# Performance work log

Hardware: AMD Instinct MI355X
Metric: run time of the kernel (lower is better)

## Reference

```python
import jax, jax.numpy as jnp
import numpy as np

N_HEAD = 16
D_MODEL = 1024
D_K = 64
D_V = 64
LN_EPS = 1e-6


def setup_inputs() -> dict:
    key = jax.random.key(0)
    ks = jax.random.split(key, 10)
    B, S = 2, 2048
    scale = 0.02
    return {
        "q": jax.random.normal(ks[0], (B, S, D_MODEL), jnp.float32),
        "k": jax.random.normal(ks[1], (B, S, D_MODEL), jnp.float32),
        "v": jax.random.normal(ks[2], (B, S, D_MODEL), jnp.float32),
        "Wq": jax.random.normal(ks[3], (D_MODEL, N_HEAD * D_K), jnp.float32) * scale,
        "Wk": jax.random.normal(ks[4], (D_MODEL, N_HEAD * D_K), jnp.float32) * scale,
        "Wv": jax.random.normal(ks[5], (D_MODEL, N_HEAD * D_V), jnp.float32) * scale,
        "Wfc": jax.random.normal(ks[6], (N_HEAD * D_V, D_MODEL), jnp.float32) * scale,
        "bfc": jnp.zeros((D_MODEL,), jnp.float32),
        "gamma": jnp.ones((D_MODEL,), jnp.float32),
        "beta": jnp.zeros((D_MODEL,), jnp.float32),
    }


def reference(q, k, v, Wq, Wk, Wv, Wfc, bfc, gamma, beta):
    B, S, _ = q.shape
    residual = q
    # QKV projections, split into heads: [B, S, H, Dh]
    qh = (q @ Wq).reshape(B, S, N_HEAD, D_K)
    kh = (k @ Wk).reshape(B, S, N_HEAD, D_K)
    vh = (v @ Wv).reshape(B, S, N_HEAD, D_V)
    # scaled dot-product attention (explicit score matrix, as in source)
    temperature = jnp.asarray(D_K, qh.dtype) ** 0.5
    attn = jnp.einsum("bqhd,bkhd->bhqk", qh, kh) / temperature
    attn = jax.nn.softmax(attn, axis=-1)
    out = jnp.einsum("bhqk,bkhd->bqhd", attn, vh).reshape(B, S, N_HEAD * D_V)
    # output projection (dropout is identity in eval mode)
    out = out @ Wfc + bfc
    # residual + layernorm (eps=1e-6)
    x = out + residual
    mu = jnp.mean(x, axis=-1, keepdims=True)
    var = jnp.mean(jnp.square(x - mu), axis=-1, keepdims=True)
    return (x - mu) / jnp.sqrt(var + LN_EPS) * gamma + beta
```

## Files before the change

kernel.cpp:

```cpp
#include <hip/hip_runtime.h>

typedef float f32x4 __attribute__((ext_vector_type(4)));
typedef short short8 __attribute__((ext_vector_type(8)));
typedef short short4v __attribute__((ext_vector_type(4)));
typedef unsigned int uint2v __attribute__((ext_vector_type(2)));
typedef unsigned short ushort_t;

#define D_MODEL 1024
#define N_HEAD 16
#define SEQ 2048
#define BATCH 2
#define M_TOK 4096
#define HD 1024
#define NT 32
#define APANEL 131072
#define WPANEL 32768
#define QSCALE_L2E 0.1803368801111f

__device__ __forceinline__ ushort_t f2bf(float f) {
    union { float f; unsigned int u; } x; x.f = f;
    unsigned int r = x.u + 0x7fffu + ((x.u >> 16) & 1u);
    return (ushort_t)(r >> 16);
}

__device__ __forceinline__ void async_copy16(const ushort_t* gptr, ushort_t* lptr) {
    __builtin_amdgcn_global_load_lds(
        (const __attribute__((address_space(1))) unsigned int*)gptr,
        (__attribute__((address_space(3))) unsigned int*)lptr, 16, 0, 0);
}

__global__ __launch_bounds__(256) void prep_fused(const float* __restrict__ w0,
                                                  const float* __restrict__ w1,
                                                  const float* __restrict__ w2,
                                                  const float* __restrict__ w3,
                                                  ushort_t* __restrict__ o0,
                                                  ushort_t* __restrict__ o1,
                                                  ushort_t* __restrict__ o2,
                                                  ushort_t* __restrict__ o3,
                                                  const float* __restrict__ q,
                                                  const float* __restrict__ k,
                                                  const float* __restrict__ v,
                                                  ushort_t* __restrict__ qo,
                                                  ushort_t* __restrict__ ko,
                                                  ushort_t* __restrict__ vo) {
    const int z = blockIdx.z;
    const int tid = threadIdx.x;
    const int flat = blockIdx.x + 64 * blockIdx.y;
    if (z < 4) {
        if (flat >= 1024) return;
        const int C = D_MODEL;
        const float* in = (z == 0) ? w0 : (z == 1) ? w1 : (z == 2) ? w2 : w3;
        ushort_t* out = (z == 0) ? o0 : (z == 1) ? o1 : (z == 2) ? o2 : o3;
        __shared__ ushort_t t[32][33];
        int bc = (flat & 31) * 32, br = (flat >> 5) * 32;
        int tx = tid & 31, ty = tid >> 5;
        for (int i = ty; i < 32; i += 8)
            t[i][tx] = f2bf(in[(size_t)(br + i) * C + bc + tx]);
        __syncthreads();
        size_t pbase = (size_t)(br >> 5) * WPANEL;
        for (int i = ty; i < 32; i += 8)
            out[pbase + (size_t)(bc + i) * 32 + tx] = t[tx][i];
    } else {
        const float* s = (z == 4) ? q : (z == 5) ? k : v;
        ushort_t* d = (z == 4) ? qo : (z == 5) ? ko : vo;
        size_t i = ((size_t)flat * 256 + tid) * 8;
        int m = (int)(i >> 10), k0 = (int)(i & 1023);
        float4 a = *(const float4*)(s + i);
        float4 b = *(const float4*)(s + i + 4);
        ushort_t tmp[8] = {f2bf(a.x), f2bf(a.y), f2bf(a.z), f2bf(a.w),
                           f2bf(b.x), f2bf(b.y), f2bf(b.z), f2bf(b.w)};
        *(short8*)(d + (size_t)(k0 >> 5) * APANEL + (size_t)m * 32 + (k0 & 31)) = *(short8*)tmp;
    }
}

__global__ __launch_bounds__(256) void gemm_qkv(const ushort_t* __restrict__ qb,
                                                const ushort_t* __restrict__ kb,
                                                const ushort_t* __restrict__ vb,
                                                const ushort_t* __restrict__ wq,
                                                const ushort_t* __restrict__ wk,
                                                const ushort_t* __restrict__ wv,
                                                ushort_t* __restrict__ Qo,
                                                ushort_t* __restrict__ Ko,
                                                ushort_t* __restrict__ V4) {
    __shared__ ushort_t As[2][128 * 32];
    __shared__ ushort_t Bs[2][128 * 32];
    const int z = blockIdx.z;
    const ushort_t* A = (z == 0) ? qb : (z == 1) ? kb : vb;
    const ushort_t* Bt = (z == 0) ? wq : (z == 1) ? wk : wv;
    const int tid = threadIdx.x;
    const int wave = tid >> 6, lane = tid & 63;
    const int quad = lane >> 4, l16 = lane & 15;
    const int m0 = blockIdx.x * 128, n0 = blockIdx.y * 128;
    const int wm = (wave >> 1) * 64, wn = (wave & 1) * 64;
    const int N = D_MODEL;

    f32x4 acc[4][4];
    for (int i = 0; i < 4; ++i)
        for (int j = 0; j < 4; ++j) acc[i][j] = (f32x4){0.f, 0.f, 0.f, 0.f};

    for (int it = 0; it < 16; ++it) {
        __syncthreads();
        const ushort_t* Ap = A + (size_t)(it * 2) * APANEL + (size_t)m0 * 32;
        const ushort_t* Bp = Bt + (size_t)(it * 2) * WPANEL + (size_t)n0 * 32;
        #pragma unroll
        for (int hf = 0; hf < 2; ++hf) {
            #pragma unroll
            for (int c = 0; c < 2; ++c) {
                int off = (wave * 2 + c) * 512;
                async_copy16(Ap + hf * APANEL + off + lane * 8, &As[hf][off] + lane * 8);
                async_copy16(Bp + hf * WPANEL + off + lane * 8, &Bs[hf][off] + lane * 8);
            }
        }
        __syncthreads();
        short8 af[4][2], bfr[4][2];
        #pragma unroll
        for (int i = 0; i < 4; ++i)
            #pragma unroll
            for (int sk = 0; sk < 2; ++sk)
                af[i][sk] = *(const short8*)&As[sk][(wm + i * 16 + l16) * 32 + quad * 8];
        #pragma unroll
        for (int j = 0; j < 4; ++j)
            #pragma unroll
            for (int sk = 0; sk < 2; ++sk)
                bfr[j][sk] = *(const short8*)&Bs[sk][(wn + j * 16 + l16) * 32 + quad * 8];
        #pragma unroll
        for (int sk = 0; sk < 2; ++sk)
            #pragma unroll
            for (int i = 0; i < 4; ++i)
                #pragma unroll
                for (int j = 0; j < 4; ++j)
                    acc[i][j] = __builtin_amdgcn_mfma_f32_16x16x32_bf16(af[i][sk], bfr[j][sk], acc[i][j], 0, 0, 0);
    }
    if (z == 2) {
        const int tile64 = m0 + wm;
        const int b2 = tile64 >> 11;
        const int kt = (tile64 & 2047) >> 6;
        #pragma unroll
        for (int i = 0; i < 4; ++i)
            #pragma unroll
            for (int j = 0; j < 4; ++j) {
                int n = n0 + wn + j * 16 + l16;
                int h2 = n >> 6, d = n & 63;
                int quadR = (quad + ((n >> 2) & 3)) & 3;
                ushort_t tmp[4];
                #pragma unroll
                for (int r = 0; r < 4; ++r) tmp[r] = f2bf(acc[i][j][r]);
                size_t dst = ((((size_t)(h2 * 2 + b2) * NT + kt) * 4 + i) << 10) + d * 16 + quadR * 4;
                *(short4v*)&V4[dst] = *(short4v*)tmp;
            }
    } else {
        ushort_t* C = (z == 0) ? Qo : Ko;
        const float scale = (z == 0) ? QSCALE_L2E : 1.0f;
        #pragma unroll
        for (int i = 0; i < 4; ++i)
            #pragma unroll
            for (int j = 0; j < 4; ++j) {
                int n = n0 + wn + j * 16 + l16;
                #pragma unroll
                for (int r = 0; r < 4; ++r) {
                    int m = m0 + wm + i * 16 + quad * 4 + r;
                    C[(size_t)m * N + n] = f2bf(acc[i][j][r] * scale);
                }
            }
    }
}

__global__ __launch_bounds__(256) void gemm_fc(const ushort_t* __restrict__ A,
                                               const ushort_t* __restrict__ Bt,
                                               float* __restrict__ Cf,
                                               const float* __restrict__ bias,
                                               const float* __restrict__ resid) {
    __shared__ ushort_t As[2][128 * 32];
    __shared__ ushort_t Bs[2][64 * 32];
    const int tid = threadIdx.x;
    const int wave = tid >> 6, lane = tid & 63;
    const int quad = lane >> 4, l16 = lane & 15;
    const int m0 = blockIdx.x * 128, n0 = blockIdx.y * 64;
    const int N = D_MODEL;

    f32x4 acc[2][4];
    for (int i = 0; i < 2; ++i)
        for (int j = 0; j < 4; ++j) acc[i][j] = (f32x4){0.f, 0.f, 0.f, 0.f};

    for (int it = 0; it < 16; ++it) {
        __syncthreads();
        const ushort_t* Ap = A + (size_t)(it * 2) * APANEL + (size_t)m0 * 32;
        const ushort_t* Bp = Bt + (size_t)(it * 2) * WPANEL + (size_t)n0 * 32;
        #pragma unroll
        for (int c = 0; c < 4; ++c) {
            int g = wave * 4 + c;
            int sk = g >> 3, off = (g & 7) * 512;
            async_copy16(Ap + sk * APANEL + off + lane * 8, &As[sk][off] + lane * 8);
        }
        #pragma unroll
        for (int c = 0; c < 2; ++c) {
            int g = wave * 2 + c;
            int sk = g >> 2, off = (g & 3) * 512;
            async_copy16(Bp + sk * WPANEL + off + lane * 8, &Bs[sk][off] + lane * 8);
        }
        __syncthreads();
        short8 af[2][2], bfr[4][2];
        #pragma unroll
        for (int i = 0; i < 2; ++i)
            #pragma unroll
            for (int sk = 0; sk < 2; ++sk)
                af[i][sk] = *(const short8*)&As[sk][(wave * 32 + i * 16 + l16) * 32 + quad * 8];
        #pragma unroll
        for (int j = 0; j < 4; ++j)
            #pragma unroll
            for (int sk = 0; sk < 2; ++sk)
                bfr[j][sk] = *(const short8*)&Bs[sk][(j * 16 + l16) * 32 + quad * 8];
        #pragma unroll
        for (int sk = 0; sk < 2; ++sk)
            #pragma unroll
            for (int i = 0; i < 2; ++i)
                #pragma unroll
                for (int j = 0; j < 4; ++j)
                    acc[i][j] = __builtin_amdgcn_mfma_f32_16x16x32_bf16(af[i][sk], bfr[j][sk], acc[i][j], 0, 0, 0);
    }
    #pragma unroll
    for (int i = 0; i < 2; ++i)
        #pragma unroll
        for (int j = 0; j < 4; ++j) {
            int n = n0 + j * 16 + l16;
            #pragma unroll
            for (int r = 0; r < 4; ++r) {
                int m = m0 + wave * 32 + i * 16 + quad * 4 + r;
                Cf[(size_t)m * N + n] = acc[i][j][r] + bias[n] + resid[(size_t)m * N + n];
            }
        }
}

__global__ __launch_bounds__(256, 3) void attn64(const ushort_t* __restrict__ Qh,
                                                 const ushort_t* __restrict__ Kh,
                                                 const ushort_t* __restrict__ V4,
                                                 ushort_t* __restrict__ O) {
    __shared__ __align__(16) char smem[25600];
    const int tid = threadIdx.x;
    const int wave = tid >> 6, lane = tid & 63;
    const int quad = lane >> 4, l16 = lane & 15;
    const int h = blockIdx.x, b = blockIdx.y, qt = blockIdx.z;
    const size_t base = (size_t)b * SEQ * HD + h * 64;
    const ushort_t* Qb = Qh + base + (size_t)(qt * 64) * HD;
    const ushort_t* Kb = Kh + base;
    const ushort_t* Vg = V4 + (((size_t)(h * 2 + b) * NT * 4) + wave) * 1024 + lane * 8;

    ushort_t* Vw = (ushort_t*)smem + wave * 3072;
    float* lsb = (float*)(smem + 24576);

    short8 qf[4][2];
    #pragma unroll
    for (int nt = 0; nt < 4; ++nt)
        #pragma unroll
        for (int s = 0; s < 2; ++s)
            qf[nt][s] = *(const short8*)(Qb + (size_t)(nt * 16 + l16) * HD + s * 32 + quad * 8);

    f32x4 oacc[4][4];
    #pragma unroll
    for (int nt = 0; nt < 4; ++nt)
        #pragma unroll
        for (int dt = 0; dt < 4; ++dt) oacc[nt][dt] = (f32x4){0.f, 0.f, 0.f, 0.f};
    float lsum[4] = {0.f, 0.f, 0.f, 0.f};

    const ushort_t* Kr = Kb + (size_t)(wave * 16 + l16) * HD + quad * 8;
    ushort_t* VLd = Vw + lane * 8;

    short8 kfA[2], kfB[2];
    #pragma unroll
    for (int s = 0; s < 2; ++s) kfA[s] = *(const short8*)(Kr + s * 32);
    #pragma unroll
    for (int c = 0; c < 2; ++c) async_copy16(Vg + c * 512, VLd + c * 512);
    #pragma unroll
    for (int s = 0; s < 2; ++s) kfB[s] = *(const short8*)(Kr + (size_t)64 * HD + s * 32);
    #pragma unroll
    for (int c = 0; c < 2; ++c) async_copy16(Vg + 4096 + c * 512, VLd + 1024 + c * 512);

    ushort_t *s0 = Vw, *s1 = Vw + 1024, *s2 = Vw + 2048;
    const int rot = (l16 >> 2) & 3;

#define ATTN_STEP(KT, KF, SUSE, SPF, WAITIMM, DO_PF)                                         \
    {                                                                                        \
        __builtin_amdgcn_s_waitcnt(WAITIMM);                                                 \
        short4v vf[4];                                                                       \
        _Pragma("unroll")                                                                    \
        for (int dt = 0; dt < 4; ++dt)                                                       \
            vf[dt] = *(const short4v*)&(SUSE)[(dt * 16 + l16) * 16 + (((quad + rot) & 3) * 4)]; \
        f32x4 sacc[4];                                                                       \
        _Pragma("unroll")                                                                    \
        for (int nt = 0; nt < 4; ++nt) sacc[nt] = (f32x4){0.f, 0.f, 0.f, 0.f};               \
        _Pragma("unroll")                                                                    \
        for (int s = 0; s < 2; ++s)                                                          \
            _Pragma("unroll")                                                                \
            for (int nt = 0; nt < 4; ++nt)                                                   \
                sacc[nt] = __builtin_amdgcn_mfma_f32_16x16x32_bf16(KF[s], qf[nt][s],         \
                                                                   sacc[nt], 0, 0, 0);       \
        if (DO_PF) {                                                                         \
            _Pragma("unroll")                                                                \
            for (int s = 0; s < 2; ++s)                                                      \
                KF[s] = *(const short8*)(Kr + (size_t)((KT) + 2) * 64 * HD + s * 32);        \
            _Pragma("unroll")                                                                \
            for (int c = 0; c < 2; ++c)                                                      \
                async_copy16(Vg + (size_t)((KT) + 2) * 4096 + c * 512,                       \
                             (SPF) + lane * 8 + c * 512);                                    \
        }                                                                                    \
        short4v pf[4];                                                                       \
        _Pragma("unroll")                                                                    \
        for (int nt = 0; nt < 4; ++nt) {                                                     \
            float p0 = __builtin_amdgcn_exp2f(sacc[nt][0]);                                  \
            float p1 = __builtin_amdgcn_exp2f(sacc[nt][1]);                                  \
            float p2 = __builtin_amdgcn_exp2f(sacc[nt][2]);                                  \
            float p3 = __builtin_amdgcn_exp2f(sacc[nt][3]);                                  \
            lsum[nt] += (p0 + p1) + (p2 + p3);                                               \
            unsigned int lo, hi;                                                             \
            asm("v_cvt_pk_bf16_f32 %0, %1, %2" : "=v"(lo) : "v"(p0), "v"(p1));               \
            asm("v_cvt_pk_bf16_f32 %0, %1, %2" : "=v"(hi) : "v"(p2), "v"(p3));               \
            uint2v pk;                                                                       \
            pk.x = lo;                                                                       \
            pk.y = hi;                                                                       \
            pf[nt] = __builtin_bit_cast(short4v, pk);                                        \
        }                                                                                    \
        _Pragma("unroll")                                                                    \
        for (int nt = 0; nt < 4; ++nt)                                                       \
            _Pragma("unroll")                                                                \
            for (int dt = 0; dt < 4; ++dt)                                                   \
                oacc[nt][dt] = __builtin_amdgcn_mfma_f32_16x16x16bf16_1k(pf[nt], vf[dt],     \
                                                                         oacc[nt][dt],       \
                                                                         0, 0, 0);           \
    }

    for (int kt0 = 0; kt0 < 30; kt0 += 2) {
        ATTN_STEP(kt0,     kfA, s0, s2, 0x0F74, true);
        ATTN_STEP(kt0 + 1, kfB, s1, s0, 0x0F74, true);
        ushort_t* t = s0; s0 = s2; s2 = s1; s1 = t;
    }
    ATTN_STEP(30, kfA, s0, s2, 0x0F74, false);
    ATTN_STEP(31, kfB, s1, s0, 0x0F70, false);
#undef ATTN_STEP

    #pragma unroll
    for (int nt = 0; nt < 4; ++nt) {
        lsum[nt] += __shfl_xor(lsum[nt], 16, 64);
        lsum[nt] += __shfl_xor(lsum[nt], 32, 64);
    }
    if (quad == 0) {
        #pragma unroll
        for (int nt = 0; nt < 4; ++nt) lsb[wave * 64 + nt * 16 + l16] = lsum[nt];
    }
    __syncthreads();

    float* R = (float*)smem;
    #pragma unroll
    for (int w = 0; w < 4; ++w) {
        if (wave == w) {
            #pragma unroll
            for (int nt = 0; nt < 4; ++nt)
                #pragma unroll
                for (int dt = 0; dt < 4; ++dt)
                    #pragma unroll
                    for (int i = 0; i < 4; ++i) {
                        int idx = (nt * 16 + quad * 4 + i) * 66 + dt * 16 + l16;
                        if (w == 0) R[idx] = oacc[nt][dt][i];
                        else        R[idx] += oacc[nt][dt][i];
                    }
        }
        __syncthreads();
    }
    float inv[4];
    #pragma unroll
    for (int i = 0; i < 4; ++i) {
        int qrow = wave * 16 + quad * 4 + i;
        float t = lsb[qrow] + lsb[64 + qrow] + lsb[128 + qrow] + lsb[192 + qrow];
        inv[i] = 1.f / t;
    }
    #pragma unroll
    for (int i = 0; i < 4; ++i) {
        int qrow = wave * 16 + quad * 4 + i;
        size_t tok = (size_t)b * SEQ + qt * 64 + qrow;
        #pragma unroll
        for (int dt = 0; dt < 4; ++dt) {
            int d = dt * 16 + l16;
            size_t dst = (size_t)(h * 2 + (dt >> 1)) * APANEL + tok * 32 + (dt & 1) * 16 + l16;
            O[dst] = f2bf(R[qrow * 66 + d] * inv[i]);
        }
    }
}

__global__ __launch_bounds__(256) void ln_kernel(float* __restrict__ x,
                                                 const float* __restrict__ gamma,
                                                 const float* __restrict__ beta) {
    const int D = D_MODEL;
    float* xr = x + (size_t)blockIdx.x * D;
    const int tid = threadIdx.x;
    float4 v = *(const float4*)(xr + tid * 4);
    float s = v.x + v.y + v.z + v.w;
    float s2 = v.x * v.x + v.y * v.y + v.z * v.z + v.w * v.w;
    #pragma unroll
    for (int off = 1; off < 64; off <<= 1) {
        s += __shfl_xor(s, off, 64);
        s2 += __shfl_xor(s2, off, 64);
    }
    __shared__ float ws1[4], ws2[4];
    int wave = tid >> 6, lane = tid & 63;
    if (lane == 0) { ws1[wave] = s; ws2[wave] = s2; }
    __syncthreads();
    s = ws1[0] + ws1[1] + ws1[2] + ws1[3];
    s2 = ws2[0] + ws2[1] + ws2[2] + ws2[3];
    float mean = s * (1.f / D);
    float var = s2 * (1.f / D) - mean * mean;
    float rstd = rsqrtf(var + 1e-6f);
    float4 g = *(const float4*)(gamma + tid * 4);
    float4 bt = *(const float4*)(beta + tid * 4);
    float4 o;
    o.x = (v.x - mean) * rstd * g.x + bt.x;
    o.y = (v.y - mean) * rstd * g.y + bt.y;
    o.z = (v.z - mean) * rstd * g.z + bt.z;
    o.w = (v.w - mean) * rstd * g.w + bt.w;
    *(float4*)(xr + tid * 4) = o;
}

extern "C" void kernel_launch(void* const* d_in, const int* in_sizes, int n_in,
                              void* d_out, int out_size, void* d_ws, size_t ws_size,
                              hipStream_t stream) {
    const float* q = (const float*)d_in[0];
    const float* k = (const float*)d_in[1];
    const float* v = (const float*)d_in[2];
    const float* Wq = (const float*)d_in[3];
    const float* Wk = (const float*)d_in[4];
    const float* Wv = (const float*)d_in[5];
    const float* Wfc = (const float*)d_in[6];
    const float* bfc = (const float*)d_in[7];
    const float* gamma = (const float*)d_in[8];
    const float* beta = (const float*)d_in[9];
    float* out = (float*)d_out;

    char* ws = (char*)d_ws;
    const size_t MB = 1u << 20;
    ushort_t* WqT  = (ushort_t*)(ws + 0 * MB);
    ushort_t* WkT  = (ushort_t*)(ws + 2 * MB);
    ushort_t* WvT  = (ushort_t*)(ws + 4 * MB);
    ushort_t* WfcT = (ushort_t*)(ws + 6 * MB);
    ushort_t* qb   = (ushort_t*)(ws + 8 * MB);
    ushort_t* kb   = (ushort_t*)(ws + 16 * MB);
    ushort_t* vb   = (ushort_t*)(ws + 24 * MB);
    ushort_t* Qh   = (ushort_t*)(ws + 32 * MB);
    ushort_t* Kh   = (ushort_t*)(ws + 40 * MB);
    ushort_t* Vt   = (ushort_t*)(ws + 48 * MB);
    ushort_t* Oh   = (ushort_t*)(ws + 8 * MB);

    const int M = M_TOK, D = D_MODEL;
    prep_fused<<<dim3(64, 32, 7), 256, 0, stream>>>(
        Wq, Wk, Wv, Wfc, WqT, WkT, WvT, WfcT, q, k, v, qb, kb, vb);

    gemm_qkv<<<dim3(M / 128, D / 128, 3), 256, 0, stream>>>(qb, kb, vb, WqT, WkT, WvT, Qh, Kh, Vt);

    attn64<<<dim3(N_HEAD, BATCH, SEQ / 64), 256, 0, stream>>>(Qh, Kh, Vt, Oh);

    gemm_fc<<<dim3(M / 128, D / 64), 256, 0, stream>>>(Oh, WfcT, out, bfc, q);

    ln_kernel<<<M, 256, 0, stream>>>(out, gamma, beta);
}
```

Measured before the change: 230.7 us.

## Software-pipeline attention PV MFMA one tile behind softmax exponentials

```diff
diff --git a/kernel.cpp b/kernel.cpp
--- a/kernel.cpp
+++ b/kernel.cpp
@@ -278,13 +278,14 @@
     ushort_t *s0 = Vw, *s1 = Vw + 1024, *s2 = Vw + 2048;
     const int rot = (l16 >> 2) & 3;
 
-#define ATTN_STEP(KT, KF, SUSE, SPF, WAITIMM, DO_PF)                                         \
+    short4v vfA[4], vfB[4], pfA[4], pfB[4];
+
+#define ATTN_STEP(KT, KF, SUSE, SPF, WAITIMM, DO_PF, VFW, PFW, VFR, PFR, DO_PV)              \
     {                                                                                        \
         __builtin_amdgcn_s_waitcnt(WAITIMM);                                                 \
-        short4v vf[4];                                                                       \
         _Pragma("unroll")                                                                    \
         for (int dt = 0; dt < 4; ++dt)                                                       \
-            vf[dt] = *(const short4v*)&(SUSE)[(dt * 16 + l16) * 16 + (((quad + rot) & 3) * 4)]; \
+            VFW[dt] = *(const short4v*)&(SUSE)[(dt * 16 + l16) * 16 + (((quad + rot) & 3) * 4)]; \
         f32x4 sacc[4];                                                                       \
         _Pragma("unroll")                                                                    \
         for (int nt = 0; nt < 4; ++nt) sacc[nt] = (f32x4){0.f, 0.f, 0.f, 0.f};               \
@@ -303,7 +304,16 @@
                 async_copy16(Vg + (size_t)((KT) + 2) * 4096 + c * 512,                       \
                              (SPF) + lane * 8 + c * 512);                                    \
         }                                                                                    \
-        short4v pf[4];                                                                       \
+        if (DO_PV) {                                                                        \
+            _Pragma("unroll")                                                                \
+            for (int nt = 0; nt < 4; ++nt)                                                   \
+                _Pragma("unroll")                                                            \
+                for (int dt = 0; dt < 4; ++dt)                                               \
+                    oacc[nt][dt] = __builtin_amdgcn_mfma_f32_16x16x16bf16_1k(PFR[nt],        \
+                                                                             VFR[dt],       \
+                                                                             oacc[nt][dt],  \
+                                                                             0, 0, 0);      \
+        }                                                                                    \
         _Pragma("unroll")                                                                    \
         for (int nt = 0; nt < 4; ++nt) {                                                     \
             float p0 = __builtin_amdgcn_exp2f(sacc[nt][0]);                                  \
@@ -317,25 +327,27 @@
             uint2v pk;                                                                       \
             pk.x = lo;                                                                       \
             pk.y = hi;                                                                       \
-            pf[nt] = __builtin_bit_cast(short4v, pk);                                        \
+            PFW[nt] = __builtin_bit_cast(short4v, pk);                                       \
         }                                                                                    \
-        _Pragma("unroll")                                                                    \
-        for (int nt = 0; nt < 4; ++nt)                                                       \
-            _Pragma("unroll")                                                                \
-            for (int dt = 0; dt < 4; ++dt)                                                   \
-                oacc[nt][dt] = __builtin_amdgcn_mfma_f32_16x16x16bf16_1k(pf[nt], vf[dt],     \
-                                                                         oacc[nt][dt],       \
-                                                                         0, 0, 0);           \
-    }
-
-    for (int kt0 = 0; kt0 < 30; kt0 += 2) {
-        ATTN_STEP(kt0,     kfA, s0, s2, 0x0F74, true);
-        ATTN_STEP(kt0 + 1, kfB, s1, s0, 0x0F74, true);
+    }
+
+    ATTN_STEP(0, kfA, s0, s2, 0x0F74, true, vfA, pfA, vfB, pfB, false);
+    ATTN_STEP(1, kfB, s1, s0, 0x0F74, true, vfB, pfB, vfA, pfA, true);
+    { ushort_t* t = s0; s0 = s2; s2 = s1; s1 = t; }
+    for (int kt0 = 2; kt0 < 30; kt0 += 2) {
+        ATTN_STEP(kt0,     kfA, s0, s2, 0x0F74, true, vfA, pfA, vfB, pfB, true);
+        ATTN_STEP(kt0 + 1, kfB, s1, s0, 0x0F74, true, vfB, pfB, vfA, pfA, true);
         ushort_t* t = s0; s0 = s2; s2 = s1; s1 = t;
     }
-    ATTN_STEP(30, kfA, s0, s2, 0x0F74, false);
-    ATTN_STEP(31, kfB, s1, s0, 0x0F70, false);
+    ATTN_STEP(30, kfA, s0, s2, 0x0F74, false, vfA, pfA, vfB, pfB, true);
+    ATTN_STEP(31, kfB, s1, s0, 0x0F70, false, vfB, pfB, vfA, pfA, true);
 #undef ATTN_STEP
+    #pragma unroll
+    for (int nt = 0; nt < 4; ++nt)
+        #pragma unroll
+        for (int dt = 0; dt < 4; ++dt)
+            oacc[nt][dt] = __builtin_amdgcn_mfma_f32_16x16x16bf16_1k(pfB[nt], vfB[dt],
+                                                                     oacc[nt][dt], 0, 0, 0);
 
     #pragma unroll
     for (int nt = 0; nt < 4; ++nt) {
```

After: 253.0 us. +9.7%, slower.
